# Performance work log

Hardware: AMD Instinct MI355X
Metric: run time of the kernel (lower is better)

Reference implementation:

```python
import jax, jax.numpy as jnp
import numpy as np

T, B = 256, 128
VOCAB, EMB, HID, LABELS = 50257, 1024, 1024, 50


def setup_inputs() -> dict:
    key = jax.random.key(0)
    ks = jax.random.split(key, 6)
    sentence = jax.random.randint(ks[0], (T, B), 0, VOCAB)
    emb = jax.random.normal(ks[1], (VOCAB, EMB), dtype=jnp.float32) * 0.02
    W = jax.random.normal(ks[2], (EMB, 3 * HID), dtype=jnp.float32) * (1.0 / np.sqrt(EMB))
    b = jnp.zeros((3 * HID,), dtype=jnp.float32)
    Wout = jax.random.normal(ks[3], (HID, LABELS), dtype=jnp.float32) * (1.0 / np.sqrt(HID))
    bout = jnp.zeros((LABELS,), dtype=jnp.float32)
    return {"sentence": sentence, "emb": emb, "W": W, "b": b, "Wout": Wout, "bout": bout}


def reference(sentence, emb, W, b, Wout, bout):
    # Embedding lookup: [T, B, EMB]
    x = emb[sentence]
    # QRNN gate projection (window=1): [T, B, 3H]
    y = jnp.einsum('tbe,eh->tbh', x, W) + b
    z, f, o = jnp.split(y, 3, axis=-1)
    z = jnp.tanh(z)
    f = jax.nn.sigmoid(f)
    o = jax.nn.sigmoid(o)

    # fo-pool recurrence: c_t = f_t * z_t + (1 - f_t) * c_{t-1}, c_0 = 0
    def step(c, zf):
        z_t, f_t = zf
        c = f_t * z_t + (1.0 - f_t) * c
        return c, c

    c0 = jnp.zeros((B, HID), dtype=z.dtype)
    _, C = jax.lax.scan(step, c0, (z, f))
    # hidden output at last timestep: h_T = o_T * c_T
    h_last = o[-1] * C[-1]  # [B, HID]
    logits = h_last @ Wout + bout  # [B, LABELS]
    return jax.nn.log_softmax(logits, axis=-1)
```

## Files before the change

kernel.cpp:

```cpp
#include <hip/hip_runtime.h>
#include <hip/hip_bf16.h>

#define T_LEN 256
#define B_DIM 128
#define EMB 1024
#define HID 1024
#define NLAB 50
#define M_ROWS (T_LEN * B_DIM)
#define N3H 3072
#define KT 16

typedef __attribute__((ext_vector_type(8))) short short8;
typedef __attribute__((ext_vector_type(4))) float f32x4;

static __device__ __forceinline__ ushort f2b(float x) {
    unsigned u = __builtin_bit_cast(unsigned, x);
    unsigned lsb = (u >> 16) & 1u;
    u += 0x7fffu + lsb;
    return (ushort)(u >> 16);
}
static __device__ __forceinline__ float b2f(ushort u) {
    unsigned v = ((unsigned)u) << 16;
    return __builtin_bit_cast(float, v);
}
static __device__ __forceinline__ void gload16(const ushort* g, ushort* l) {
    __builtin_amdgcn_global_load_lds(
        (const __attribute__((address_space(1))) unsigned int*)g,
        (__attribute__((address_space(3))) unsigned int*)l,
        16, 0, 0);
}
static __device__ __forceinline__ float fast_sigmoid(float y) {
    return 1.f / (1.f + __expf(-y));
}
static __device__ __forceinline__ float fast_tanh(float y) {
    float e = __expf(2.f * y);
    return (e - 1.f) / (e + 1.f);
}

__global__ __launch_bounds__(256) void prep(
    const int* __restrict__ sent, const float* __restrict__ emb,
    const float* __restrict__ W,
    ushort* __restrict__ xb, ushort* __restrict__ Wt)
{
    __shared__ float tile[32][33];
    const int wg = blockIdx.x;
    if (wg < 2048) {
        const int row = wg * 16 + (threadIdx.x >> 4);
        const int seg = threadIdx.x & 15;
        const size_t src = (size_t)sent[row] * EMB;
        const float4* ep = (const float4*)(emb + src);
        ushort4* op = (ushort4*)(xb + (size_t)row * EMB);
#pragma unroll
        for (int j = 0; j < 16; j++) {
            float4 v = ep[seg + j * 16];
            ushort4 o;
            o.x = f2b(v.x); o.y = f2b(v.y); o.z = f2b(v.z); o.w = f2b(v.w);
            op[seg + j * 16] = o;
        }
    } else {
        const int bx = wg - 2048;
        const int n0 = (bx % 96) * 32, k0 = (bx / 96) * 32;
        const int tx = threadIdx.x & 31, ty = threadIdx.x >> 5;
#pragma unroll
        for (int j = 0; j < 32; j += 8)
            tile[ty + j][tx] = W[(size_t)(k0 + ty + j) * N3H + n0 + tx];
        __syncthreads();
#pragma unroll
        for (int j = 0; j < 32; j += 8)
            Wt[(size_t)(n0 + ty + j) * EMB + k0 + tx] = f2b(tile[tx][ty + j]);
    }
}

__global__ __launch_bounds__(256) void gemm128(
    const ushort* __restrict__ A, const ushort* __restrict__ Bt,
    const float* __restrict__ bias,
    ushort* __restrict__ zb, ushort* __restrict__ fb, ushort* __restrict__ ob)
{
    __shared__ ushort LA[128 * 64];
    __shared__ ushort LB[128 * 64];

    const int tid = threadIdx.x;
    const int lane = tid & 63;
    const int w = tid >> 6;
    const int wr = w >> 1, wc = w & 1;
    const int l15 = lane & 15, lh = lane >> 4;

    const int wg = blockIdx.x;
    const ushort *Ab, *Bb;
    const float* bptr;
    ushort* dst;
    int rowbase, colbase;
    bool use_tanh;
    if (wg < 4096) {
        const int w2 = (wg & 7) * 512 + (wg >> 3);
        const int mt = w2 >> 4, nt = w2 & 15;
        Ab = A + (size_t)mt * 128 * EMB;
        Bb = Bt + (size_t)nt * 128 * EMB;
        bptr = bias + nt * 128;
        rowbase = mt * 128;
        if (nt < 8) { dst = zb; colbase = nt * 128; use_tanh = true; }
        else        { dst = fb; colbase = (nt - 8) * 128; use_tanh = false; }
    } else {
        const int q = wg - 4096;
        Ab = A + (size_t)(M_ROWS - 128) * EMB;
        Bb = Bt + (size_t)(2048 + q * 128) * EMB;
        bptr = bias + 2048 + q * 128;
        rowbase = 0; colbase = q * 128;
        dst = ob; use_tanh = false;
    }

    const ushort* gA[4];
    const ushort* gB[4];
    int dOf[4];
#pragma unroll
    for (int q = 0; q < 4; q++) {
        const int c = q * 256 + tid;
        const int row = c >> 3;
        const int gsrc = (c & 7) ^ (row & 7);
        gA[q] = Ab + (size_t)row * EMB + gsrc * 8;
        gB[q] = Bb + (size_t)row * EMB + gsrc * 8;
        dOf[q] = c * 8;
    }

    const int swz0 = (lh ^ (l15 & 7)) * 8;
    const int swz1 = ((4 + lh) ^ (l15 & 7)) * 8;
    const int aRow = (wr * 64 + l15) * 64;
    const int bRow = (wc * 64 + l15) * 64;

    f32x4 acc[4][4] = {};

    for (int kk = 0; kk < KT; ++kk) {
        const int ko = kk * 64;
        gload16(gA[0] + ko, LA + dOf[0]);
        gload16(gA[1] + ko, LA + dOf[1]);
        gload16(gA[2] + ko, LA + dOf[2]);
        gload16(gA[3] + ko, LA + dOf[3]);
        gload16(gB[0] + ko, LB + dOf[0]);
        gload16(gB[1] + ko, LB + dOf[1]);
        gload16(gB[2] + ko, LB + dOf[2]);
        gload16(gB[3] + ko, LB + dOf[3]);
        __syncthreads();

        {
            short8 a0 = *(const short8*)&LA[aRow + swz0];
            short8 a1 = *(const short8*)&LA[aRow + 1024 + swz0];
            short8 a2 = *(const short8*)&LA[aRow + 2048 + swz0];
            short8 a3 = *(const short8*)&LA[aRow + 3072 + swz0];
            short8 b0 = *(const short8*)&LB[bRow + swz0];
            short8 b1 = *(const short8*)&LB[bRow + 1024 + swz0];
            short8 b2 = *(const short8*)&LB[bRow + 2048 + swz0];
            short8 b3 = *(const short8*)&LB[bRow + 3072 + swz0];
#pragma unroll
            for (int mi = 0; mi < 4; mi++) {
                const short8 am = (mi == 0) ? a0 : (mi == 1) ? a1 : (mi == 2) ? a2 : a3;
                acc[mi][0] = __builtin_amdgcn_mfma_f32_16x16x32_bf16(am, b0, acc[mi][0], 0, 0, 0);
                acc[mi][1] = __builtin_amdgcn_mfma_f32_16x16x32_bf16(am, b1, acc[mi][1], 0, 0, 0);
                acc[mi][2] = __builtin_amdgcn_mfma_f32_16x16x32_bf16(am, b2, acc[mi][2], 0, 0, 0);
                acc[mi][3] = __builtin_amdgcn_mfma_f32_16x16x32_bf16(am, b3, acc[mi][3], 0, 0, 0);
            }
        }
        {
            short8 a0 = *(const short8*)&LA[aRow + swz1];
            short8 a1 = *(const short8*)&LA[aRow + 1024 + swz1];
            short8 a2 = *(const short8*)&LA[aRow + 2048 + swz1];
            short8 a3 = *(const short8*)&LA[aRow + 3072 + swz1];
            short8 b0 = *(const short8*)&LB[bRow + swz1];
            short8 b1 = *(const short8*)&LB[bRow + 1024 + swz1];
            short8 b2 = *(const short8*)&LB[bRow + 2048 + swz1];
            short8 b3 = *(const short8*)&LB[bRow + 3072 + swz1];
#pragma unroll
            for (int mi = 0; mi < 4; mi++) {
                const short8 am = (mi == 0) ? a0 : (mi == 1) ? a1 : (mi == 2) ? a2 : a3;
                acc[mi][0] = __builtin_amdgcn_mfma_f32_16x16x32_bf16(am, b0, acc[mi][0], 0, 0, 0);
                acc[mi][1] = __builtin_amdgcn_mfma_f32_16x16x32_bf16(am, b1, acc[mi][1], 0, 0, 0);
                acc[mi][2] = __builtin_amdgcn_mfma_f32_16x16x32_bf16(am, b2, acc[mi][2], 0, 0, 0);
                acc[mi][3] = __builtin_amdgcn_mfma_f32_16x16x32_bf16(am, b3, acc[mi][3], 0, 0, 0);
            }
        }
        __syncthreads();
    }

#pragma unroll
    for (int mi = 0; mi < 4; mi++) {
#pragma unroll
        for (int ni = 0; ni < 4; ni++) {
            const int nb = wc * 64 + ni * 16 + l15;
            const float bv = bptr[nb];
            const int rl = wr * 64 + mi * 16 + lh * 4;
#pragma unroll
            for (int r = 0; r < 4; r++) {
                float y = acc[mi][ni][r] + bv;
                float a = use_tanh ? fast_tanh(y) : fast_sigmoid(y);
                dst[(size_t)(rowbase + rl + r) * HID + colbase + nb] = f2b(a);
            }
        }
    }
}

__global__ __launch_bounds__(256) void fo_pool(
    const unsigned* __restrict__ z32, const unsigned* __restrict__ fz32,
    const unsigned* __restrict__ o32, float* __restrict__ hbuf)
{
    const int p = blockIdx.x * 256 + threadIdx.x;
    float c0 = 0.f, c1 = 0.f;
#pragma unroll 8
    for (int t = 0; t < T_LEN; ++t) {
        unsigned zz = z32[(size_t)t * (B_DIM * HID / 2) + p];
        unsigned ff = fz32[(size_t)t * (B_DIM * HID / 2) + p];
        float z0 = b2f((ushort)(zz & 0xffffu)), z1 = b2f((ushort)(zz >> 16));
        float f0 = b2f((ushort)(ff & 0xffffu)), f1 = b2f((ushort)(ff >> 16));
        c0 += f0 * (z0 - c0);
        c1 += f1 * (z1 - c1);
    }
    unsigned oo = o32[p];
    float o0 = b2f((ushort)(oo & 0xffffu)), o1 = b2f((ushort)(oo >> 16));
    hbuf[2 * p]     = o0 * c0;
    hbuf[2 * p + 1] = o1 * c1;
}

__global__ __launch_bounds__(64) void classify(
    const float* __restrict__ hbuf, const float* __restrict__ Wout,
    const float* __restrict__ bout, float* __restrict__ out)
{
    __shared__ float hs[HID];
    const int b = blockIdx.x, l = threadIdx.x;
#pragma unroll
    for (int j = 0; j < HID; j += 64) hs[j + l] = hbuf[(size_t)b * HID + j + l];
    __syncthreads();
    float acc = -1e30f;
    if (l < NLAB) {
        float s = bout[l];
#pragma unroll 4
        for (int e = 0; e < HID; e++) s += hs[e] * Wout[(size_t)e * NLAB + l];
        acc = s;
    }
    float m = acc;
#pragma unroll
    for (int off = 32; off; off >>= 1) m = fmaxf(m, __shfl_xor(m, off));
    float ex = (l < NLAB) ? expf(acc - m) : 0.f;
    float sum = ex;
#pragma unroll
    for (int off = 32; off; off >>= 1) sum += __shfl_xor(sum, off);
    if (l < NLAB) out[(size_t)b * NLAB + l] = acc - m - logf(sum);
}

extern "C" void kernel_launch(void* const* d_in, const int* in_sizes, int n_in,
                              void* d_out, int out_size, void* d_ws, size_t ws_size,
                              hipStream_t stream) {
    const int* sent = (const int*)d_in[0];
    const float* emb = (const float*)d_in[1];
    const float* W = (const float*)d_in[2];
    const float* bias = (const float*)d_in[3];
    const float* Wout = (const float*)d_in[4];
    const float* bout = (const float*)d_in[5];
    float* out = (float*)d_out;

    ushort* xb = (ushort*)d_ws;
    ushort* Wt = xb + (size_t)M_ROWS * EMB;
    ushort* zb = Wt + (size_t)N3H * EMB;
    ushort* fb = zb + (size_t)M_ROWS * HID;
    ushort* ob = fb + (size_t)M_ROWS * HID;
    float* hb = (float*)(ob + (size_t)B_DIM * HID);

    hipLaunchKernelGGL(prep, dim3(2048 + 3072), dim3(256), 0, stream,
                       sent, emb, W, xb, Wt);
    hipLaunchKernelGGL(gemm128, dim3(4096 + 8), dim3(256), 0, stream,
                       xb, Wt, bias, zb, fb, ob);
    hipLaunchKernelGGL(fo_pool, dim3(B_DIM * HID / 2 / 256), dim3(256), 0, stream,
                       (const unsigned*)zb, (const unsigned*)fb,
                       (const unsigned*)ob, hb);
    hipLaunchKernelGGL(classify, dim3(B_DIM), dim3(64), 0, stream,
                       hb, Wout, bout, out);
}
```

Baseline: 323.7 us.

## Split fo-pool recurrence into time segments with parallel scan combine

```diff
diff --git a/kernel.cpp b/kernel.cpp
--- a/kernel.cpp
+++ b/kernel.cpp
@@ -9,6 +9,9 @@
 #define M_ROWS (T_LEN * B_DIM)
 #define N3H 3072
 #define KT 16
+#define NPAIR (B_DIM * HID / 2)
+#define NSEG 4
+#define SEG_T (T_LEN / NSEG)
 
 typedef __attribute__((ext_vector_type(8))) short short8;
 typedef __attribute__((ext_vector_type(4))) float f32x4;
@@ -44,21 +47,21 @@
 {
     __shared__ float tile[32][33];
     const int wg = blockIdx.x;
-    if (wg < 2048) {
-        const int row = wg * 16 + (threadIdx.x >> 4);
-        const int seg = threadIdx.x & 15;
+    if (wg < 4096) {
+        const int row = wg * 8 + (threadIdx.x >> 5);
+        const int seg = threadIdx.x & 31;
         const size_t src = (size_t)sent[row] * EMB;
         const float4* ep = (const float4*)(emb + src);
         ushort4* op = (ushort4*)(xb + (size_t)row * EMB);
 #pragma unroll
-        for (int j = 0; j < 16; j++) {
-            float4 v = ep[seg + j * 16];
+        for (int j = 0; j < 8; j++) {
+            float4 v = ep[seg + j * 32];
             ushort4 o;
             o.x = f2b(v.x); o.y = f2b(v.y); o.z = f2b(v.z); o.w = f2b(v.w);
-            op[seg + j * 16] = o;
+            op[seg + j * 32] = o;
         }
     } else {
-        const int bx = wg - 2048;
+        const int bx = wg - 4096;
         const int n0 = (bx % 96) * 32, k0 = (bx / 96) * 32;
         const int tx = threadIdx.x & 31, ty = threadIdx.x >> 5;
 #pragma unroll
@@ -197,20 +200,40 @@
     }
 }
 
-__global__ __launch_bounds__(256) void fo_pool(
+__global__ __launch_bounds__(256) void fo_seg(
     const unsigned* __restrict__ z32, const unsigned* __restrict__ fz32,
-    const unsigned* __restrict__ o32, float* __restrict__ hbuf)
+    float4* __restrict__ segAB)
+{
+    const int s = blockIdx.x >> 8;
+    const int p = (blockIdx.x & 255) * 256 + threadIdx.x;
+    float A0 = 1.f, A1 = 1.f, B0 = 0.f, B1 = 0.f;
+    const int t0 = s * SEG_T;
+#pragma unroll 8
+    for (int t = t0; t < t0 + SEG_T; ++t) {
+        unsigned zz = z32[(size_t)t * NPAIR + p];
+        unsigned ff = fz32[(size_t)t * NPAIR + p];
+        float z0 = b2f((ushort)(zz & 0xffffu)), z1 = b2f((ushort)(zz >> 16));
+        float f0 = b2f((ushort)(ff & 0xffffu)), f1 = b2f((ushort)(ff >> 16));
+        B0 += f0 * (z0 - B0);
+        B1 += f1 * (z1 - B1);
+        A0 *= (1.f - f0);
+        A1 *= (1.f - f1);
+    }
+    float4 v; v.x = A0; v.y = A1; v.z = B0; v.w = B1;
+    segAB[(size_t)s * NPAIR + p] = v;
+}
+
+__global__ __launch_bounds__(256) void fo_combine(
+    const float4* __restrict__ segAB, const unsigned* __restrict__ o32,
+    float* __restrict__ hbuf)
 {
     const int p = blockIdx.x * 256 + threadIdx.x;
     float c0 = 0.f, c1 = 0.f;
-#pragma unroll 8
-    for (int t = 0; t < T_LEN; ++t) {
-        unsigned zz = z32[(size_t)t * (B_DIM * HID / 2) + p];
-        unsigned ff = fz32[(size_t)t * (B_DIM * HID / 2) + p];
-        float z0 = b2f((ushort)(zz & 0xffffu)), z1 = b2f((ushort)(zz >> 16));
-        float f0 = b2f((ushort)(ff & 0xffffu)), f1 = b2f((ushort)(ff >> 16));
-        c0 += f0 * (z0 - c0);
-        c1 += f1 * (z1 - c1);
+#pragma unroll
+    for (int s = 0; s < NSEG; ++s) {
+        float4 v = segAB[(size_t)s * NPAIR + p];
+        c0 = v.x * c0 + v.z;
+        c1 = v.y * c1 + v.w;
     }
     unsigned oo = o32[p];
     float o0 = b2f((ushort)(oo & 0xffffu)), o1 = b2f((ushort)(oo >> 16));
@@ -261,14 +284,16 @@
     ushort* fb = zb + (size_t)M_ROWS * HID;
     ushort* ob = fb + (size_t)M_ROWS * HID;
     float* hb = (float*)(ob + (size_t)B_DIM * HID);
-
-    hipLaunchKernelGGL(prep, dim3(2048 + 3072), dim3(256), 0, stream,
+    float4* segAB = (float4*)xb;
+
+    hipLaunchKernelGGL(prep, dim3(4096 + 3072), dim3(256), 0, stream,
                        sent, emb, W, xb, Wt);
     hipLaunchKernelGGL(gemm128, dim3(4096 + 8), dim3(256), 0, stream,
                        xb, Wt, bias, zb, fb, ob);
-    hipLaunchKernelGGL(fo_pool, dim3(B_DIM * HID / 2 / 256), dim3(256), 0, stream,
-                       (const unsigned*)zb, (const unsigned*)fb,
-                       (const unsigned*)ob, hb);
+    hipLaunchKernelGGL(fo_seg, dim3(NSEG * 256), dim3(256), 0, stream,
+                       (const unsigned*)zb, (const unsigned*)fb, segAB);
+    hipLaunchKernelGGL(fo_combine, dim3(NPAIR / 256), dim3(256), 0, stream,
+                       segAB, (const unsigned*)ob, hb);
     hipLaunchKernelGGL(classify, dim3(B_DIM), dim3(64), 0, stream,
                        hb, Wout, bout, out);
 }
```

Result: no change. 323.2 us (-0.1%).
